# Kernel optimization log

Hardware: AMD Instinct MI355X
Metric: run time of the kernel (lower is better)

The kernel has to match this reference:

```python
import jax, jax.numpy as jnp
from jax import lax
import numpy as np
import math

D = 96   # d_model
H = 4    # num_heads (d_k = d_v = D per head, per the source)
K = 7    # depthwise kernel size
L = 4    # num conv layers


def _pos_encoding(seq_len, d):
    # Faithful to the source's (nonstandard) exponents: sin uses 2*i/d, cos uses 2*(i+1)/d
    pos = np.arange(seq_len, dtype=np.float32)[:, None]
    i = np.arange(0, d, 2, dtype=np.float32)
    pe = np.zeros((seq_len, d), dtype=np.float32)
    pe[:, 0::2] = np.sin(pos / 10000.0 ** (2.0 * i / d))
    pe[:, 1::2] = np.cos(pos / 10000.0 ** (2.0 * (i + 1.0) / d))
    return jnp.asarray(pe)


def _layernorm(x, g, b, eps=1e-5):
    m = jnp.mean(x, axis=-1, keepdims=True)
    v = jnp.mean((x - m) ** 2, axis=-1, keepdims=True)
    return (x - m) / jnp.sqrt(v + eps) * g + b


def setup_inputs() -> dict:
    key = jax.random.key(0)
    ks = jax.random.split(key, 10)
    B, S = 128, 384

    def xavier(k, shape, fan_in, fan_out):
        bound = math.sqrt(6.0 / (fan_in + fan_out))
        return jax.random.uniform(k, shape, jnp.float32, -bound, bound)

    return {
        "input": jax.random.normal(ks[0], (B, S, D), jnp.float32),
        "mask": jnp.zeros((B, S), dtype=bool),
        "conv_dw": jax.random.normal(ks[1], (L, D, 1, K), jnp.float32) * 0.05,
        "conv_dw_b": jnp.zeros((L, D), jnp.float32),
        "conv_pw": jax.random.normal(ks[2], (L, D, D, 1), jnp.float32) * 0.05,
        "conv_pw_b": jnp.zeros((L, D), jnp.float32),
        "WQ": xavier(ks[3], (H, D, D), D, D),
        "WK": xavier(ks[4], (H, D, D), D, D),
        "WV": xavier(ks[5], (H, D, D), D, D),
        "WO": xavier(ks[6], (H * D, D), H * D, D),
        "ffn_w1": jax.random.normal(ks[7], (D, D // 2), jnp.float32) * 0.1,
        "ffn_b1": jnp.zeros((D // 2,), jnp.float32),
        "ffn_w2": jax.random.normal(ks[8], (D // 2, D), jnp.float32) * 0.1,
        "ffn_b2": jnp.zeros((D,), jnp.float32),
        "ln_g": jnp.ones((L + 2, D), jnp.float32),
        "ln_b": jnp.zeros((L + 2, D), jnp.float32),
    }


def reference(input, mask, conv_dw, conv_dw_b, conv_pw, conv_pw_b,
              WQ, WK, WV, WO, ffn_w1, ffn_b1, ffn_w2, ffn_b2, ln_g, ln_b):
    B, S, _ = input.shape
    dn = ("NCH", "OIH", "NCH")

    # positional encoding (eval mode: all dropout is identity)
    x = input * jnp.float32(math.sqrt(D)) + _pos_encoding(S, D)[None]

    # conv blocks: LN -> depthwise conv -> pointwise conv -> relu -> residual
    for i in range(L):
        h = _layernorm(x, ln_g[i], ln_b[i])
        h = jnp.transpose(h, (0, 2, 1))  # [B, C, S]
        h = lax.conv_general_dilated(h, conv_dw[i], (1,), "SAME",
                                     feature_group_count=D, dimension_numbers=dn)
        h = h + conv_dw_b[i][None, :, None]
        h = lax.conv_general_dilated(h, conv_pw[i], (1,), "SAME", dimension_numbers=dn)
        h = jax.nn.relu(h + conv_pw_b[i][None, :, None])
        x = x + jnp.transpose(h, (0, 2, 1))

    # multi-head attention with per-head full-width projections (d_k = D)
    h = _layernorm(x, ln_g[L], ln_b[L])
    Q = jnp.einsum("bsd,hde->hbse", h, WQ)
    Kh = jnp.einsum("bsd,hde->hbse", h, WK)
    V = jnp.einsum("bsd,hde->hbse", h, WV)
    # source divides scores by temperature = 1/sqrt(d_k) => multiply by sqrt(D)
    scores = jnp.einsum("hbqe,hbke->hbqk", Q, Kh) * jnp.float32(math.sqrt(D))
    # mask is viewed [B, S, 1]: masks query rows, broadcast over keys
    scores = jnp.where(mask[None, :, :, None], -jnp.inf, scores)
    attn = jax.nn.softmax(scores, axis=-1)
    ctx = jnp.einsum("hbqk,hbke->hbqe", attn, V)
    cat = jnp.transpose(ctx, (1, 2, 0, 3)).reshape(B, S, H * D)
    x = x + cat @ WO

    # feed-forward: Linear -> sigmoid -> Linear, residual
    h2 = _layernorm(x, ln_g[L + 1], ln_b[L + 1])
    ff = jax.nn.sigmoid(h2 @ ffn_w1 + ffn_b1) @ ffn_w2 + ffn_b2
    return x + ff
```

## Files before the change

### kernel.cpp

```cpp
#include <hip/hip_runtime.h>
#include <math.h>


constexpr int B = 128;
constexpr int S = 384;
constexpr int D = 96;
constexpr int H = 4;
constexpr int KW = 7;
constexpr int L = 4;
constexpr int ROWS = B * S;
constexpr long long NTOT = (long long)ROWS * D;
constexpr float SQRTD = 9.797958971132712f;
constexpr float LOG2E = 1.4426950408889634f;

typedef _Float16 f16x8 __attribute__((ext_vector_type(8)));
typedef float f32x4 __attribute__((ext_vector_type(4)));
typedef unsigned short us;
typedef unsigned short us4 __attribute__((ext_vector_type(4)));
typedef unsigned short us8 __attribute__((ext_vector_type(8)));

__device__ __forceinline__ us f2h(float f) {
    _Float16 h = (_Float16)f;
    return __builtin_bit_cast(us, h);
}
__device__ __forceinline__ f16x8 ldh(const us* p) {
    return *reinterpret_cast<const f16x8*>(p);
}

__global__ void pe_kernel(float* __restrict__ pe) {
    int idx = blockIdx.x * 256 + threadIdx.x;
    if (idx >= S * D) return;
    int s = idx / D, c = idx - s * D;
    int j = c >> 1;
    float expo = (c & 1) ? (4.0f * j + 2.0f) / 96.0f : (4.0f * j) / 96.0f;
    float freq = expf(-expo * logf(10000.0f));
    float ang = (float)s * freq;
    pe[idx] = (c & 1) ? cosf(ang) : sinf(ang);
}

__global__ void prep_w(const float* __restrict__ WQ, const float* __restrict__ WK,
                       const float* __restrict__ cpw, const float* __restrict__ w1,
                       const float* __restrict__ w2,
                       us* __restrict__ wqS, us* __restrict__ wkS, us* __restrict__ pwS,
                       us* __restrict__ w1S, us* __restrict__ w2S) {
    int idx = blockIdx.x * 256 + threadIdx.x;
    if (idx >= H * D * D) return;
    int h = idx / (D * D), rem = idx - h * (D * D);
    int d = rem / D, e = rem - d * D;
    int n = e >> 4, lmod = e & 15, kk = d >> 5, ldiv = (d >> 3) & 3, j = d & 7;
    size_t fi = (size_t)(((n * 3 + kk) * 64 + ldiv * 16 + lmod) * 8 + j);
    wqS[(size_t)h * D * D + fi] = f2h(WQ[idx] * SQRTD * LOG2E);
    wkS[(size_t)h * D * D + fi] = f2h(WK[idx]);
    {
        int l = idx / (D * D);
        int o = rem / D, c = rem - o * D;
        int no = o >> 4, lo = o & 15, kc = c >> 5, lc = (c >> 3) & 3, jc = c & 7;
        pwS[(size_t)l * D * D + (size_t)(((no * 3 + kc) * 64 + lc * 16 + lo) * 8 + jc)] =
            f2h(cpw[idx]);
    }
    if (idx < 48 * 96) {
        int m = idx / 96, c = idx - m * 96;
        int nm = m >> 4, lm = m & 15, kc = c >> 5, lc = (c >> 3) & 3, jc = c & 7;
        w1S[((nm * 3 + kc) * 64 + lc * 16 + lm) * 8 + jc] = f2h(w1[c * 48 + m]);
    }
    if (idx < 96 * 64) {
        int o = idx / 64, mk = idx - o * 64;
        int no = o >> 4, lo = o & 15, km = mk >> 5, lm2 = (mk >> 3) & 3, jm = mk & 7;
        w2S[((no * 2 + km) * 64 + lm2 * 16 + lo) * 8 + jm] =
            (mk < 48) ? f2h(w2[mk * 96 + o]) : (us)0;
    }
}

__global__ void prep_wvo(const float* __restrict__ WV, const float* __restrict__ WO,
                         us* __restrict__ wvoS) {
    int blk = blockIdx.x;
    int h = blk / 6, ot = blk - h * 6;
    int tid = threadIdx.x;
    const float* wv = WV + (size_t)h * D * D;
    const float* wo = WO + (size_t)h * D * D;
    for (int i = tid; i < 16 * 96; i += 256) {
        int lmod = i / 96, d = i - (i / 96) * 96;
        int o = ot * 16 + lmod;
        float acc = 0.f;
        for (int e = 0; e < 96; e++) acc += wv[d * 96 + e] * wo[e * 96 + o];
        int kk = d >> 5, ldiv = (d >> 3) & 3, j = d & 7;
        wvoS[(size_t)h * D * D + (size_t)(((ot * 3 + kk) * 64 + ldiv * 16 + lmod) * 8 + j)] =
            f2h(acc);
    }
}

__global__ void conv0f(const float* __restrict__ in, const float* __restrict__ pe,
                       const float* __restrict__ g0, const float* __restrict__ b0,
                       float* __restrict__ xout, us* __restrict__ lnout,
                       const float* __restrict__ dwW, const float* __restrict__ dwB,
                       const us* __restrict__ pwW, const float* __restrict__ pwb,
                       const float* __restrict__ gnext, const float* __restrict__ bnext) {
    __shared__ us lnb_s[70 * 104];
    __shared__ us dwb_s[64 * 104];
    __shared__ float lw[96 * 8];
    int tid = threadIdx.x;
    int wave = tid >> 6, lane = tid & 63;
    int r0 = blockIdx.x * 64;
    int b = r0 / S, s0 = r0 % S;

    for (int i = tid; i < 96 * KW; i += 256) lw[(i / KW) * 8 + (i % KW)] = dwW[i];

    for (int i = wave; i < 70; i += 4) {
        int s = s0 - 3 + i;
        bool valid = (unsigned)s < (unsigned)S;
        float v0 = 0.f, v1 = 0.f;
        if (valid) {
            size_t ro = ((size_t)b * S + s) * 96;
            v0 = in[ro + lane] * SQRTD + pe[s * 96 + lane];
            v1 = (lane < 32) ? in[ro + 64 + lane] * SQRTD + pe[s * 96 + 64 + lane] : 0.f;
        }
        float sm = v0 + v1, q = v0 * v0 + v1 * v1;
        for (int off = 32; off > 0; off >>= 1) {
            sm += __shfl_xor(sm, off);
            q += __shfl_xor(q, off);
        }
        float mean = sm * (1.0f / D);
        float var = q * (1.0f / D) - mean * mean;
        float rstd = rsqrtf(var + 1e-5f);
        lnb_s[i * 104 + lane] = f2h(valid ? (v0 - mean) * rstd * g0[lane] + b0[lane] : 0.f);
        if (lane < 32)
            lnb_s[i * 104 + 64 + lane] =
                f2h(valid ? (v1 - mean) * rstd * g0[lane + 64] + b0[lane + 64] : 0.f);
    }
    __syncthreads();

    for (int u = tid; u < 768; u += 256) {
        int j = u / 12, c0 = (u - (u / 12) * 12) * 8;
        float acc[8];
        #pragma unroll
        for (int j2 = 0; j2 < 8; j2++) acc[j2] = dwB[c0 + j2];
        #pragma unroll
        for (int k = 0; k < KW; k++) {
            f16x8 v = ldh(&lnb_s[(j + k) * 104 + c0]);
            #pragma unroll
            for (int j2 = 0; j2 < 8; j2++) acc[j2] += (float)v[j2] * lw[(c0 + j2) * 8 + k];
        }
        us8 o;
        #pragma unroll
        for (int j2 = 0; j2 < 8; j2++) o[j2] = f2h(acc[j2]);
        *reinterpret_cast<us8*>(&dwb_s[j * 104 + c0]) = o;
    }
    __syncthreads();

    int lmod = lane & 15, ldiv = lane >> 4, m0 = wave * 16;
    f32x4 acc[6] = {};
    #pragma unroll
    for (int kk = 0; kk < 3; kk++) {
        f16x8 af = ldh(&dwb_s[(m0 + lmod) * 104 + kk * 32 + ldiv * 8]);
        #pragma unroll
        for (int n = 0; n < 6; n++) {
            f16x8 bf = ldh(pwW + (size_t)((n * 3 + kk) * 64) * 8 + lane * 8);
            acc[n] = __builtin_amdgcn_mfma_f32_16x16x32_f16(af, bf, acc[n], 0, 0, 0);
        }
    }

    float gv[6], bv2[6], pb[6];
    #pragma unroll
    for (int n = 0; n < 6; n++) {
        int o = n * 16 + lmod;
        gv[n] = gnext[o];
        bv2[n] = bnext[o];
        pb[n] = pwb[o];
    }
    #pragma unroll
    for (int n = 0; n < 6; n++) {
        int o = n * 16 + lmod;
        #pragma unroll
        for (int r = 0; r < 4; r++) {
            int sr = m0 + ldiv * 4 + r;
            size_t row = (size_t)r0 + sr;
            float base = in[row * 96 + o] * SQRTD + pe[(s0 + sr) * 96 + o];
            acc[n][r] = base + fmaxf(acc[n][r] + pb[n], 0.f);
        }
    }
    #pragma unroll
    for (int r = 0; r < 4; r++) {
        float sm = 0.f, qq = 0.f;
        #pragma unroll
        for (int n = 0; n < 6; n++) {
            sm += acc[n][r];
            qq += acc[n][r] * acc[n][r];
        }
        #pragma unroll
        for (int st = 1; st <= 8; st <<= 1) {
            sm += __shfl_xor(sm, st);
            qq += __shfl_xor(qq, st);
        }
        float mean = sm * (1.0f / D);
        float var = qq * (1.0f / D) - mean * mean;
        float rstd = rsqrtf(var + 1e-5f);
        size_t row = (size_t)r0 + m0 + ldiv * 4 + r;
        #pragma unroll
        for (int n = 0; n < 6; n++) {
            int o = n * 16 + lmod;
            xout[row * 96 + o] = acc[n][r];
            lnout[row * 96 + o] = f2h((acc[n][r] - mean) * rstd * gv[n] + bv2[n]);
        }
    }
}

__global__ void conv2(const float* __restrict__ xin, const us* __restrict__ lnin,
                      float* __restrict__ xout, us* __restrict__ lnout,
                      const float* __restrict__ dwW, const float* __restrict__ dwB,
                      const us* __restrict__ pwW, const float* __restrict__ pwb,
                      const float* __restrict__ gnext, const float* __restrict__ bnext) {
    __shared__ us dwb_s[64 * 104];
    __shared__ float lw[96 * 8];
    int tid = threadIdx.x;
    int wave = tid >> 6, lane = tid & 63;
    int r0 = blockIdx.x * 64;
    int b = r0 / S, s0 = r0 % S;

    for (int i = tid; i < 96 * KW; i += 256) lw[(i / KW) * 8 + (i % KW)] = dwW[i];
    __syncthreads();

    for (int u = tid; u < 768; u += 256) {
        int j = u / 12, c0 = (u - (u / 12) * 12) * 8;
        float acc[8];
        #pragma unroll
        for (int j2 = 0; j2 < 8; j2++) acc[j2] = dwB[c0 + j2];
        #pragma unroll
        for (int k = 0; k < KW; k++) {
            int ss = s0 + j + k - 3;
            if ((unsigned)ss < (unsigned)S) {
                f16x8 v = ldh(lnin + ((size_t)b * S + ss) * 96 + c0);
                #pragma unroll
                for (int j2 = 0; j2 < 8; j2++) acc[j2] += (float)v[j2] * lw[(c0 + j2) * 8 + k];
            }
        }
        us8 o;
        #pragma unroll
        for (int j2 = 0; j2 < 8; j2++) o[j2] = f2h(acc[j2]);
        *reinterpret_cast<us8*>(&dwb_s[j * 104 + c0]) = o;
    }
    __syncthreads();

    int lmod = lane & 15, ldiv = lane >> 4, m0 = wave * 16;
    f32x4 acc[6] = {};
    #pragma unroll
    for (int kk = 0; kk < 3; kk++) {
        f16x8 af = ldh(&dwb_s[(m0 + lmod) * 104 + kk * 32 + ldiv * 8]);
        #pragma unroll
        for (int n = 0; n < 6; n++) {
            f16x8 bf = ldh(pwW + (size_t)((n * 3 + kk) * 64) * 8 + lane * 8);
            acc[n] = __builtin_amdgcn_mfma_f32_16x16x32_f16(af, bf, acc[n], 0, 0, 0);
        }
    }

    float gv[6], bv2[6], pb[6];
    #pragma unroll
    for (int n = 0; n < 6; n++) {
        int o = n * 16 + lmod;
        gv[n] = gnext[o];
        bv2[n] = bnext[o];
        pb[n] = pwb[o];
    }
    #pragma unroll
    for (int n = 0; n < 6; n++) {
        #pragma unroll
        for (int r = 0; r < 4; r++) {
            size_t row = (size_t)r0 + m0 + ldiv * 4 + r;
            acc[n][r] = xin[row * 96 + n * 16 + lmod] + fmaxf(acc[n][r] + pb[n], 0.f);
        }
    }
    #pragma unroll
    for (int r = 0; r < 4; r++) {
        float sm = 0.f, qq = 0.f;
        #pragma unroll
        for (int n = 0; n < 6; n++) {
            sm += acc[n][r];
            qq += acc[n][r] * acc[n][r];
        }
        #pragma unroll
        for (int st = 1; st <= 8; st <<= 1) {
            sm += __shfl_xor(sm, st);
            qq += __shfl_xor(qq, st);
        }
        float mean = sm * (1.0f / D);
        float var = qq * (1.0f / D) - mean * mean;
        float rstd = rsqrtf(var + 1e-5f);
        size_t row = (size_t)r0 + m0 + ldiv * 4 + r;
        #pragma unroll
        for (int n = 0; n < 6; n++) {
            int o = n * 16 + lmod;
            xout[row * 96 + o] = acc[n][r];
            lnout[row * 96 + o] = f2h((acc[n][r] - mean) * rstd * gv[n] + bv2[n]);
        }
    }
}

__global__ void conv3p(const float* __restrict__ xin, const us* __restrict__ lnin,
                       float* __restrict__ xout, us* __restrict__ lnout,
                       const float* __restrict__ dwW, const float* __restrict__ dwB,
                       const us* __restrict__ pwW, const float* __restrict__ pwb,
                       const float* __restrict__ gnext, const float* __restrict__ bnext,
                       const us* __restrict__ wkS, const us* __restrict__ wvoS,
                       us* __restrict__ Kall, us* __restrict__ Vall) {
    __shared__ float lw[96 * 8];
    __shared__ us stg[96 * 72];
    __shared__ us lnstg[64 * 104];
    int tid = threadIdx.x;
    int wave = tid >> 6, lane = tid & 63;
    int lmod = lane & 15, ldiv = lane >> 4, m0 = wave * 16;
    int r0 = blockIdx.x * 64;
    int b = r0 / S, s0 = r0 % S;

    for (int i = tid; i < 96 * KW; i += 256) lw[(i / KW) * 8 + (i % KW)] = dwW[i];
    __syncthreads();

    for (int u = tid; u < 768; u += 256) {
        int j = u / 12, c0 = (u - (u / 12) * 12) * 8;
        float acc[8];
        #pragma unroll
        for (int j2 = 0; j2 < 8; j2++) acc[j2] = dwB[c0 + j2];
        #pragma unroll
        for (int k = 0; k < KW; k++) {
            int ss = s0 + j + k - 3;
            if ((unsigned)ss < (unsigned)S) {
                f16x8 v = ldh(lnin + ((size_t)b * S + ss) * 96 + c0);
                #pragma unroll
                for (int j2 = 0; j2 < 8; j2++) acc[j2] += (float)v[j2] * lw[(c0 + j2) * 8 + k];
            }
        }
        us8 o;
        #pragma unroll
        for (int j2 = 0; j2 < 8; j2++) o[j2] = f2h(acc[j2]);
        *reinterpret_cast<us8*>(&stg[j * 104 + c0]) = o;
    }
    __syncthreads();

    f32x4 acc[6] = {};
    #pragma unroll
    for (int kk = 0; kk < 3; kk++) {
        f16x8 af = ldh(&stg[(m0 + lmod) * 104 + kk * 32 + ldiv * 8]);
        #pragma unroll
        for (int n = 0; n < 6; n++) {
            f16x8 bf = ldh(pwW + (size_t)((n * 3 + kk) * 64) * 8 + lane * 8);
            acc[n] = __builtin_amdgcn_mfma_f32_16x16x32_f16(af, bf, acc[n], 0, 0, 0);
        }
    }

    float gv[6], bv2[6], pb[6];
    #pragma unroll
    for (int n = 0; n < 6; n++) {
        int o = n * 16 + lmod;
        gv[n] = gnext[o];
        bv2[n] = bnext[o];
        pb[n] = pwb[o];
    }
    #pragma unroll
    for (int n = 0; n < 6; n++) {
        #pragma unroll
        for (int r = 0; r < 4; r++) {
            size_t row = (size_t)r0 + m0 + ldiv * 4 + r;
            acc[n][r] = xin[row * 96 + n * 16 + lmod] + fmaxf(acc[n][r] + pb[n], 0.f);
        }
    }
    #pragma unroll
    for (int r = 0; r < 4; r++) {
        float sm = 0.f, qq = 0.f;
        #pragma unroll
        for (int n = 0; n < 6; n++) {
            sm += acc[n][r];
            qq += acc[n][r] * acc[n][r];
        }
        #pragma unroll
        for (int st = 1; st <= 8; st <<= 1) {
            sm += __shfl_xor(sm, st);
            qq += __shfl_xor(qq, st);
        }
        float mean = sm * (1.0f / D);
        float var = qq * (1.0f / D) - mean * mean;
        float rstd = rsqrtf(var + 1e-5f);
        size_t row = (size_t)r0 + m0 + ldiv * 4 + r;
        #pragma unroll
        for (int n = 0; n < 6; n++) {
            int o = n * 16 + lmod;
            xout[row * 96 + o] = acc[n][r];
            us hv = f2h((acc[n][r] - mean) * rstd * gv[n] + bv2[n]);
            lnout[row * 96 + o] = hv;
            lnstg[(m0 + ldiv * 4 + r) * 104 + o] = hv;
        }
    }
    __syncthreads();

    f16x8 af[3];
    #pragma unroll
    for (int kk = 0; kk < 3; kk++)
        af[kk] = ldh(&lnstg[(m0 + lmod) * 104 + kk * 32 + ldiv * 8]);

    for (int hd = 0; hd < H; hd++) {
        f32x4 ka[6] = {};
        #pragma unroll
        for (int kk = 0; kk < 3; kk++)
            #pragma unroll
            for (int n = 0; n < 6; n++) {
                f16x8 bf = ldh(wkS + (size_t)hd * D * D + (size_t)((n * 3 + kk) * 64) * 8 + lane * 8);
                ka[n] = __builtin_amdgcn_mfma_f32_16x16x32_f16(af[kk], bf, ka[n], 0, 0, 0);
            }
        __syncthreads();
        us* kT = stg + wave * 1664;
        #pragma unroll
        for (int n = 0; n < 6; n++)
            #pragma unroll
            for (int r = 0; r < 4; r++)
                kT[(ldiv * 4 + r) * 104 + n * 16 + lmod] = f2h(ka[n][r]);
        int t0 = (r0 % S) / 16 + wave;
        us* dst = Kall + (size_t)hd * NTOT + ((size_t)(b * 24 + t0) * 3) * 512;
        #pragma unroll
        for (int kk = 0; kk < 3; kk++) {
            us8 v = *reinterpret_cast<const us8*>(&kT[lmod * 104 + kk * 32 + ldiv * 8]);
            *reinterpret_cast<us8*>(dst + kk * 512 + lane * 8) = v;
        }
        f32x4 va[6] = {};
        #pragma unroll
        for (int kk = 0; kk < 3; kk++)
            #pragma unroll
            for (int n = 0; n < 6; n++) {
                f16x8 bf =
                    ldh(wvoS + (size_t)hd * D * D + (size_t)((n * 3 + kk) * 64) * 8 + lane * 8);
                va[n] = __builtin_amdgcn_mfma_f32_16x16x32_f16(af[kk], bf, va[n], 0, 0, 0);
            }
        __syncthreads();
        #pragma unroll
        for (int n = 0; n < 6; n++)
            #pragma unroll
            for (int r = 0; r < 4; r++)
                stg[(n * 16 + lmod) * 72 + m0 + ldiv * 4 + r] = f2h(va[n][r]);
        __syncthreads();
        int cblk = (r0 % S) / 64;
        us* dsth = Vall + (size_t)hd * NTOT;
        #pragma unroll
        for (int n = 0; n < 6; n++)
            #pragma unroll
            for (int kk = 0; kk < 2; kk++) {
                us8 v =
                    *reinterpret_cast<const us8*>(&stg[(n * 16 + lmod) * 72 + kk * 32 + ldiv * 8]);
                *reinterpret_cast<us8*>(
                    dsth + ((size_t)((b * 6 + cblk) * 6 + n) * 2 + kk) * 512 + lane * 8) = v;
            }
    }
}

__global__ __launch_bounds__(256, 2) void attn_g(const us* __restrict__ h16,
                                                 const us* __restrict__ wqS,
                                                 const us* __restrict__ Kall,
                                                 const us* __restrict__ Vall,
                                                 us* __restrict__ xpart) {
    __shared__ us pool[38400];
    int tid = threadIdx.x, wave = tid >> 6, lane = tid & 63;
    int lmod = lane & 15, ldiv = lane >> 4;
    int p = blockIdx.x;
    int gl = (p & 7) * 128 + (p >> 3);
    int qt = gl & 1;
    int bh = gl >> 1;
    int b = bh >> 2, hd = bh & 3;
    size_t rowbase = (size_t)b * S + qt * 192 + wave * 48;

    const us* Kh = Kall + (size_t)hd * NTOT + (size_t)b * 24 * 1536;
    const us* Vh = Vall + (size_t)hd * NTOT + (size_t)b * 36 * 1024;
    us* P = pool + 24576 + wave * 3456;

    us8 k0s[3];
    #pragma unroll
    for (int j = 0; j < 3; j++)
        k0s[j] = *reinterpret_cast<const us8*>(Kh + (size_t)(j * 256 + tid) * 8);

    f32x4 qa0[6] = {}, qa1[6] = {}, qa2[6] = {};
    #pragma unroll
    for (int kk = 0; kk < 3; kk++) {
        f16x8 a0 = ldh(h16 + (rowbase + lmod) * 96 + kk * 32 + ldiv * 8);
        f16x8 a1 = ldh(h16 + (rowbase + 16 + lmod) * 96 + kk * 32 + ldiv * 8);
        f16x8 a2 = ldh(h16 + (rowbase + 32 + lmod) * 96 + kk * 32 + ldiv * 8);
        #pragma unroll
        for (int n = 0; n < 6; n++) {
            f16x8 bf = ldh(wqS + (size_t)hd * D * D + (size_t)((n * 3 + kk) * 64) * 8 + lane * 8);
            qa0[n] = __builtin_amdgcn_mfma_f32_16x16x32_f16(a0, bf, qa0[n], 0, 0, 0);
            qa1[n] = __builtin_amdgcn_mfma_f32_16x16x32_f16(a1, bf, qa1[n], 0, 0, 0);
            qa2[n] = __builtin_amdgcn_mfma_f32_16x16x32_f16(a2, bf, qa2[n], 0, 0, 0);
        }
    }
    us* qst = pool + wave * 4992;
    #pragma unroll
    for (int n = 0; n < 6; n++)
        #pragma unroll
        for (int r = 0; r < 4; r++) {
            qst[(ldiv * 4 + r) * 104 + n * 16 + lmod] = f2h(qa0[n][r]);
            qst[(16 + ldiv * 4 + r) * 104 + n * 16 + lmod] = f2h(qa1[n][r]);
            qst[(32 + ldiv * 4 + r) * 104 + n * 16 + lmod] = f2h(qa2[n][r]);
        }
    f16x8 aq0[3], aq1[3], aq2[3];
    #pragma unroll
    for (int kk = 0; kk < 3; kk++) {
        aq0[kk] = ldh(&qst[lmod * 104 + kk * 32 + ldiv * 8]);
        aq1[kk] = ldh(&qst[(16 + lmod) * 104 + kk * 32 + ldiv * 8]);
        aq2[kk] = ldh(&qst[(32 + lmod) * 104 + kk * 32 + ldiv * 8]);
    }
    __syncthreads();
    #pragma unroll
    for (int j = 0; j < 3; j++)
        *reinterpret_cast<us8*>(&pool[(j * 256 + tid) * 8]) = k0s[j];
    __syncthreads();

    float mx0 = -1e30f, mx1 = -1e30f, mx2 = -1e30f;
    for (int c = 0; c < 6; c++) {
        us* kbc = pool + (c & 1) * 6144;
        us8 kn[3], vn[3];
        bool last = (c == 5);
        if (!last) {
            const us* src = Kh + (size_t)(c + 1) * 6144;
            #pragma unroll
            for (int j = 0; j < 3; j++)
                kn[j] = *reinterpret_cast<const us8*>(src + (size_t)(j * 256 + tid) * 8);
        } else {
            #pragma unroll
            for (int j = 0; j < 3; j++) {
                kn[j] = *reinterpret_cast<const us8*>(Kh + (size_t)(j * 256 + tid) * 8);
                vn[j] = *reinterpret_cast<const us8*>(Vh + (size_t)(j * 256 + tid) * 8);
            }
        }
        __builtin_amdgcn_s_setprio(1);
        f32x4 s0[4] = {}, s1[4] = {}, s2[4] = {};
        #pragma unroll
        for (int nt = 0; nt < 4; nt++)
            #pragma unroll
            for (int kk = 0; kk < 3; kk++) {
                f16x8 bf = ldh(&kbc[(nt * 3 + kk) * 512 + lane * 8]);
                s0[nt] = __builtin_amdgcn_mfma_f32_16x16x32_f16(bf, aq0[kk], s0[nt], 0, 0, 0);
                s1[nt] = __builtin_amdgcn_mfma_f32_16x16x32_f16(bf, aq1[kk], s1[nt], 0, 0, 0);
                s2[nt] = __builtin_amdgcn_mfma_f32_16x16x32_f16(bf, aq2[kk], s2[nt], 0, 0, 0);
            }
        __builtin_amdgcn_s_setprio(0);
        #pragma unroll
        for (int nt = 0; nt < 4; nt++)
            #pragma unroll
            for (int r = 0; r < 4; r++) {
                mx0 = fmaxf(mx0, s0[nt][r]);
                mx1 = fmaxf(mx1, s1[nt][r]);
                mx2 = fmaxf(mx2, s2[nt][r]);
            }
        us* kbw = pool + (last ? 0 : ((c & 1) ^ 1)) * 6144;
        #pragma unroll
        for (int j = 0; j < 3; j++)
            *reinterpret_cast<us8*>(&kbw[(j * 256 + tid) * 8]) = kn[j];
        if (last) {
            #pragma unroll
            for (int j = 0; j < 3; j++)
                *reinterpret_cast<us8*>(&pool[12288 + (j * 256 + tid) * 8]) = vn[j];
        }
        __syncthreads();
    }
    mx0 = fmaxf(mx0, __shfl_xor(mx0, 16));
    mx0 = fmaxf(mx0, __shfl_xor(mx0, 32));
    mx1 = fmaxf(mx1, __shfl_xor(mx1, 16));
    mx1 = fmaxf(mx1, __shfl_xor(mx1, 32));
    mx2 = fmaxf(mx2, __shfl_xor(mx2, 16));
    mx2 = fmaxf(mx2, __shfl_xor(mx2, 32));

    f32x4 oacc0[6] = {}, oacc1[6] = {}, oacc2[6] = {};
    float l0 = 0.f, l1 = 0.f, l2 = 0.f;
    for (int c = 0; c < 6; c++) {
        us* kbc = pool + (c & 1) * 6144;
        us* vbc = pool + 12288 + (c & 1) * 6144;
        us8 kn[3], vn[3];
        if (c < 5) {
            const us* ksrc = Kh + (size_t)(c + 1) * 6144;
            const us* vsrc = Vh + (size_t)(c + 1) * 6144;
            #pragma unroll
            for (int j = 0; j < 3; j++) {
                kn[j] = *reinterpret_cast<const us8*>(ksrc + (size_t)(j * 256 + tid) * 8);
                vn[j] = *reinterpret_cast<const us8*>(vsrc + (size_t)(j * 256 + tid) * 8);
            }
        }
        __builtin_amdgcn_s_setprio(1);
        f32x4 s0[4] = {}, s1[4] = {}, s2[4] = {};
        #pragma unroll
        for (int nt = 0; nt < 4; nt++)
            #pragma unroll
            for (int kk = 0; kk < 3; kk++) {
                f16x8 bf = ldh(&kbc[(nt * 3 + kk) * 512 + lane * 8]);
                s0[nt] = __builtin_amdgcn_mfma_f32_16x16x32_f16(bf, aq0[kk], s0[nt], 0, 0, 0);
                s1[nt] = __builtin_amdgcn_mfma_f32_16x16x32_f16(bf, aq1[kk], s1[nt], 0, 0, 0);
                s2[nt] = __builtin_amdgcn_mfma_f32_16x16x32_f16(bf, aq2[kk], s2[nt], 0, 0, 0);
            }
        __builtin_amdgcn_s_setprio(0);
        #pragma unroll
        for (int nt = 0; nt < 4; nt++) {
            us4 pk0, pk1, pk2;
            #pragma unroll
            for (int r = 0; r < 4; r++) {
                float p0 = exp2f(s0[nt][r] - mx0);
                float p1 = exp2f(s1[nt][r] - mx1);
                float p2 = exp2f(s2[nt][r] - mx2);
                l0 += p0;
                l1 += p1;
                l2 += p2;
                pk0[r] = f2h(p0);
                pk1[r] = f2h(p1);
                pk2[r] = f2h(p2);
            }
            int kc = nt * 16 + ldiv * 4;
            *reinterpret_cast<us4*>(&P[lmod * 72 + kc]) = pk0;
            *reinterpret_cast<us4*>(&P[(16 + lmod) * 72 + kc]) = pk1;
            *reinterpret_cast<us4*>(&P[(32 + lmod) * 72 + kc]) = pk2;
        }
        __builtin_amdgcn_s_setprio(1);
        #pragma unroll
        for (int kk = 0; kk < 2; kk++) {
            f16x8 pf0 = ldh(&P[lmod * 72 + kk * 32 + ldiv * 8]);
            f16x8 pf1 = ldh(&P[(16 + lmod) * 72 + kk * 32 + ldiv * 8]);
            f16x8 pf2 = ldh(&P[(32 + lmod) * 72 + kk * 32 + ldiv * 8]);
            #pragma unroll
            for (int n = 0; n < 6; n++) {
                f16x8 bf = ldh(&vbc[(n * 2 + kk) * 512 + lane * 8]);
                oacc0[n] = __builtin_amdgcn_mfma_f32_16x16x32_f16(pf0, bf, oacc0[n], 0, 0, 0);
                oacc1[n] = __builtin_amdgcn_mfma_f32_16x16x32_f16(pf1, bf, oacc1[n], 0, 0, 0);
                oacc2[n] = __builtin_amdgcn_mfma_f32_16x16x32_f16(pf2, bf, oacc2[n], 0, 0, 0);
            }
        }
        __builtin_amdgcn_s_setprio(0);
        if (c < 5) {
            us* kbn = pool + ((c & 1) ^ 1) * 6144;
            us* vbn = pool + 12288 + ((c & 1) ^ 1) * 6144;
            #pragma unroll
            for (int j = 0; j < 3; j++) {
                *reinterpret_cast<us8*>(&kbn[(j * 256 + tid) * 8]) = kn[j];
                *reinterpret_cast<us8*>(&vbn[(j * 256 + tid) * 8]) = vn[j];
            }
            __syncthreads();
        }
    }
    l0 += __shfl_xor(l0, 16);
    l0 += __shfl_xor(l0, 32);
    l1 += __shfl_xor(l1, 16);
    l1 += __shfl_xor(l1, 32);
    l2 += __shfl_xor(l2, 16);
    l2 += __shfl_xor(l2, 32);

    us* xp = xpart + (size_t)hd * NTOT;
    #pragma unroll
    for (int r = 0; r < 4; r++) {
        int srcl = ldiv * 4 + r;
        float inv0 = 1.f / __shfl(l0, srcl);
        float inv1 = 1.f / __shfl(l1, srcl);
        float inv2 = 1.f / __shfl(l2, srcl);
        #pragma unroll
        for (int n = 0; n < 6; n++) {
            xp[(rowbase + ldiv * 4 + r) * 96 + n * 16 + lmod] = f2h(oacc0[n][r] * inv0);
            xp[(rowbase + 16 + ldiv * 4 + r) * 96 + n * 16 + lmod] = f2h(oacc1[n][r] * inv1);
            xp[(rowbase + 32 + ldiv * 4 + r) * 96 + n * 16 + lmod] = f2h(oacc2[n][r] * inv2);
        }
    }
}

__global__ void ffn_ln(const float* __restrict__ x, const us* __restrict__ xpart,
                       const float* __restrict__ gln, const float* __restrict__ bln,
                       const us* __restrict__ w1S, const float* __restrict__ b1,
                       const us* __restrict__ w2S, const float* __restrict__ b2,
                       float* __restrict__ out) {
    __shared__ float xf[64 * 96];
    __shared__ us lnb[64 * 104];
    __shared__ us mid[64 * 72];
    int tid = threadIdx.x, wave = tid >> 6, lane = tid & 63;
    int lmod = lane & 15, ldiv = lane >> 4, m0 = wave * 16;
    int row0 = blockIdx.x * 64;

    for (int i = wave; i < 64; i += 4) {
        size_t ro = (size_t)(row0 + i) * 96;
        float v0 = x[ro + lane];
        float v1 = (lane < 32) ? x[ro + 64 + lane] : 0.f;
        #pragma unroll
        for (int h = 0; h < H; h++) {
            const us* xp = xpart + (size_t)h * NTOT + ro;
            v0 += (float)__builtin_bit_cast(_Float16, xp[lane]);
            if (lane < 32) v1 += (float)__builtin_bit_cast(_Float16, xp[64 + lane]);
        }
        xf[i * 96 + lane] = v0;
        if (lane < 32) xf[i * 96 + 64 + lane] = v1;
        float sm = v0 + v1, q = v0 * v0 + v1 * v1;
        for (int off = 32; off > 0; off >>= 1) {
            sm += __shfl_xor(sm, off);
            q += __shfl_xor(q, off);
        }
        float mean = sm * (1.0f / D);
        float var = q * (1.0f / D) - mean * mean;
        float rstd = rsqrtf(var + 1e-5f);
        lnb[i * 104 + lane] = f2h((v0 - mean) * rstd * gln[lane] + bln[lane]);
        if (lane < 32)
            lnb[i * 104 + 64 + lane] = f2h((v1 - mean) * rstd * gln[lane + 64] + bln[lane + 64]);
    }
    __syncthreads();

    f32x4 a3[3] = {};
    #pragma unroll
    for (int kk = 0; kk < 3; kk++) {
        f16x8 af = ldh(&lnb[(m0 + lmod) * 104 + kk * 32 + ldiv * 8]);
        #pragma unroll
        for (int n = 0; n < 3; n++) {
            f16x8 bf = ldh(w1S + (size_t)((n * 3 + kk) * 64) * 8 + lane * 8);
            a3[n] = __builtin_amdgcn_mfma_f32_16x16x32_f16(af, bf, a3[n], 0, 0, 0);
        }
    }
    #pragma unroll
    for (int n = 0; n < 3; n++) {
        float bv = b1[n * 16 + lmod];
        #pragma unroll
        for (int r = 0; r < 4; r++) {
            float v = a3[n][r] + bv;
            mid[(m0 + ldiv * 4 + r) * 72 + n * 16 + lmod] = f2h(1.f / (1.f + __expf(-v)));
        }
    }
    #pragma unroll
    for (int r = 0; r < 4; r++) mid[(m0 + ldiv * 4 + r) * 72 + 48 + lmod] = 0;
    __syncthreads();

    f32x4 a6[6] = {};
    #pragma unroll
    for (int kk = 0; kk < 2; kk++) {
        f16x8 af = ldh(&mid[(m0 + lmod) * 72 + kk * 32 + ldiv * 8]);
        #pragma unroll
        for (int n = 0; n < 6; n++) {
            f16x8 bf = ldh(w2S + (size_t)((n * 2 + kk) * 64) * 8 + lane * 8);
            a6[n] = __builtin_amdgcn_mfma_f32_16x16x32_f16(af, bf, a6[n], 0, 0, 0);
        }
    }
    #pragma unroll
    for (int n = 0; n < 6; n++) {
        int o = n * 16 + lmod;
        float bv = b2[o];
        #pragma unroll
        for (int r = 0; r < 4; r++) {
            int sr = m0 + ldiv * 4 + r;
            out[(size_t)(row0 + sr) * 96 + o] = xf[sr * 96 + o] + a6[n][r] + bv;
        }
    }
}

extern "C" void kernel_launch(void* const* d_in, const int* in_sizes, int n_in,
                              void* d_out, int out_size, void* d_ws, size_t ws_size,
                              hipStream_t stream) {
    const float* in   = (const float*)d_in[0];
    const float* cdw  = (const float*)d_in[2];
    const float* cdwb = (const float*)d_in[3];
    const float* cpw  = (const float*)d_in[4];
    const float* cpwb = (const float*)d_in[5];
    const float* WQ   = (const float*)d_in[6];
    const float* WK   = (const float*)d_in[7];
    const float* WV   = (const float*)d_in[8];
    const float* WO   = (const float*)d_in[9];
    const float* w1   = (const float*)d_in[10];
    const float* b1   = (const float*)d_in[11];
    const float* w2   = (const float*)d_in[12];
    const float* b2   = (const float*)d_in[13];
    const float* lng  = (const float*)d_in[14];
    const float* lnb  = (const float*)d_in[15];
    float* out = (float*)d_out;
    float* ws = (float*)d_ws;

    float* xA  = ws;
    float* xB  = xA + NTOT;
    float* pe  = xB + NTOT;
    us* lnA    = (us*)(pe + S * D);
    us* lnB    = lnA + NTOT;
    us* Kall   = lnB + NTOT;
    us* Vall   = Kall + (size_t)H * NTOT;
    us* xpart  = Vall + (size_t)H * NTOT;
    us* wqS    = xpart + (size_t)H * NTOT;
    us* wkS    = wqS + H * D * D;
    us* wvoS   = wkS + H * D * D;
    us* pwS    = wvoS + H * D * D;
    us* w1S    = pwS + L * D * D;
    us* w2S    = w1S + 48 * 96;

    pe_kernel<<<(S * D + 255) / 256, 256, 0, stream>>>(pe);
    prep_w<<<(H * D * D + 255) / 256, 256, 0, stream>>>(WQ, WK, cpw, w1, w2,
                                                        wqS, wkS, pwS, w1S, w2S);
    prep_wvo<<<H * 6, 256, 0, stream>>>(WV, WO, wvoS);

    conv0f<<<ROWS / 64, 256, 0, stream>>>(in, pe, lng, lnb, xA, lnB,
                                          cdw, cdwb, pwS, cpwb, lng + D, lnb + D);
    conv2<<<ROWS / 64, 256, 0, stream>>>(xA, lnB, xB, lnA, cdw + D * KW, cdwb + D,
                                         pwS + D * D, cpwb + D, lng + 2 * D, lnb + 2 * D);
    conv2<<<ROWS / 64, 256, 0, stream>>>(xB, lnA, xA, lnB, cdw + 2 * D * KW, cdwb + 2 * D,
                                         pwS + 2 * D * D, cpwb + 2 * D, lng + 3 * D,
                                         lnb + 3 * D);
    conv3p<<<ROWS / 64, 256, 0, stream>>>(xA, lnB, xB, lnA, cdw + 3 * D * KW, cdwb + 3 * D,
                                          pwS + 3 * D * D, cpwb + 3 * D, lng + 4 * D,
                                          lnb + 4 * D, wkS, wvoS, Kall, Vall);

    attn_g<<<1024, 256, 0, stream>>>(lnA, wqS, Kall, Vall, xpart);

    ffn_ln<<<ROWS / 64, 256, 0, stream>>>(xB, xpart, lng + 5 * D, lnb + 5 * D,
                                          w1S, b1, w2S, b2, out);
}
```

Baseline: 274.6 us.

## Replace two-pass softmax with single-pass online softmax in attention kernel

Removes the separate first pass over all key chunks that computed the row maximum, and instead keeps a running maximum with rescaling of the accumulated sum and output, as in flash attention. This halves the QK^T MFMA work and the K loads and LDS traffic for that pass. In exchange each chunk adds cross-lane shuffles for the chunk max and the per-row scale factors, plus multiplies to rescale the output accumulators. The first V chunk is now prefetched alongside the first K chunk.

Result: no change. 272.8 us (-0.7%).

```diff
diff --git a/kernel.cpp b/kernel.cpp
--- a/kernel.cpp
+++ b/kernel.cpp
@@ -466,10 +466,12 @@
     const us* Vh = Vall + (size_t)hd * NTOT + (size_t)b * 36 * 1024;
     us* P = pool + 24576 + wave * 3456;
 
-    us8 k0s[3];
-    #pragma unroll
-    for (int j = 0; j < 3; j++)
+    us8 k0s[3], v0s[3];
+    #pragma unroll
+    for (int j = 0; j < 3; j++) {
         k0s[j] = *reinterpret_cast<const us8*>(Kh + (size_t)(j * 256 + tid) * 8);
+        v0s[j] = *reinterpret_cast<const us8*>(Vh + (size_t)(j * 256 + tid) * 8);
+    }
 
     f32x4 qa0[6] = {}, qa1[6] = {}, qa2[6] = {};
     #pragma unroll
@@ -503,67 +505,15 @@
     }
     __syncthreads();
     #pragma unroll
-    for (int j = 0; j < 3; j++)
+    for (int j = 0; j < 3; j++) {
         *reinterpret_cast<us8*>(&pool[(j * 256 + tid) * 8]) = k0s[j];
-    __syncthreads();
-
-    float mx0 = -1e30f, mx1 = -1e30f, mx2 = -1e30f;
-    for (int c = 0; c < 6; c++) {
-        us* kbc = pool + (c & 1) * 6144;
-        us8 kn[3], vn[3];
-        bool last = (c == 5);
-        if (!last) {
-            const us* src = Kh + (size_t)(c + 1) * 6144;
-            #pragma unroll
-            for (int j = 0; j < 3; j++)
-                kn[j] = *reinterpret_cast<const us8*>(src + (size_t)(j * 256 + tid) * 8);
-        } else {
-            #pragma unroll
-            for (int j = 0; j < 3; j++) {
-                kn[j] = *reinterpret_cast<const us8*>(Kh + (size_t)(j * 256 + tid) * 8);
-                vn[j] = *reinterpret_cast<const us8*>(Vh + (size_t)(j * 256 + tid) * 8);
-            }
-        }
-        __builtin_amdgcn_s_setprio(1);
-        f32x4 s0[4] = {}, s1[4] = {}, s2[4] = {};
-        #pragma unroll
-        for (int nt = 0; nt < 4; nt++)
-            #pragma unroll
-            for (int kk = 0; kk < 3; kk++) {
-                f16x8 bf = ldh(&kbc[(nt * 3 + kk) * 512 + lane * 8]);
-                s0[nt] = __builtin_amdgcn_mfma_f32_16x16x32_f16(bf, aq0[kk], s0[nt], 0, 0, 0);
-                s1[nt] = __builtin_amdgcn_mfma_f32_16x16x32_f16(bf, aq1[kk], s1[nt], 0, 0, 0);
-                s2[nt] = __builtin_amdgcn_mfma_f32_16x16x32_f16(bf, aq2[kk], s2[nt], 0, 0, 0);
-            }
-        __builtin_amdgcn_s_setprio(0);
-        #pragma unroll
-        for (int nt = 0; nt < 4; nt++)
-            #pragma unroll
-            for (int r = 0; r < 4; r++) {
-                mx0 = fmaxf(mx0, s0[nt][r]);
-                mx1 = fmaxf(mx1, s1[nt][r]);
-                mx2 = fmaxf(mx2, s2[nt][r]);
-            }
-        us* kbw = pool + (last ? 0 : ((c & 1) ^ 1)) * 6144;
-        #pragma unroll
-        for (int j = 0; j < 3; j++)
-            *reinterpret_cast<us8*>(&kbw[(j * 256 + tid) * 8]) = kn[j];
-        if (last) {
-            #pragma unroll
-            for (int j = 0; j < 3; j++)
-                *reinterpret_cast<us8*>(&pool[12288 + (j * 256 + tid) * 8]) = vn[j];
-        }
-        __syncthreads();
-    }
-    mx0 = fmaxf(mx0, __shfl_xor(mx0, 16));
-    mx0 = fmaxf(mx0, __shfl_xor(mx0, 32));
-    mx1 = fmaxf(mx1, __shfl_xor(mx1, 16));
-    mx1 = fmaxf(mx1, __shfl_xor(mx1, 32));
-    mx2 = fmaxf(mx2, __shfl_xor(mx2, 16));
-    mx2 = fmaxf(mx2, __shfl_xor(mx2, 32));
-
+        *reinterpret_cast<us8*>(&pool[12288 + (j * 256 + tid) * 8]) = v0s[j];
+    }
+    __syncthreads();
+
+    float m0v = -1e30f, m1v = -1e30f, m2v = -1e30f;
+    float l0 = 0.f, l1 = 0.f, l2 = 0.f;
     f32x4 oacc0[6] = {}, oacc1[6] = {}, oacc2[6] = {};
-    float l0 = 0.f, l1 = 0.f, l2 = 0.f;
     for (int c = 0; c < 6; c++) {
         us* kbc = pool + (c & 1) * 6144;
         us* vbc = pool + 12288 + (c & 1) * 6144;
@@ -589,14 +539,50 @@
                 s2[nt] = __builtin_amdgcn_mfma_f32_16x16x32_f16(bf, aq2[kk], s2[nt], 0, 0, 0);
             }
         __builtin_amdgcn_s_setprio(0);
+        float cm0 = -1e30f, cm1 = -1e30f, cm2 = -1e30f;
+        #pragma unroll
+        for (int nt = 0; nt < 4; nt++)
+            #pragma unroll
+            for (int r = 0; r < 4; r++) {
+                cm0 = fmaxf(cm0, s0[nt][r]);
+                cm1 = fmaxf(cm1, s1[nt][r]);
+                cm2 = fmaxf(cm2, s2[nt][r]);
+            }
+        cm0 = fmaxf(cm0, __shfl_xor(cm0, 16));
+        cm0 = fmaxf(cm0, __shfl_xor(cm0, 32));
+        cm1 = fmaxf(cm1, __shfl_xor(cm1, 16));
+        cm1 = fmaxf(cm1, __shfl_xor(cm1, 32));
+        cm2 = fmaxf(cm2, __shfl_xor(cm2, 16));
+        cm2 = fmaxf(cm2, __shfl_xor(cm2, 32));
+        float mn0 = fmaxf(m0v, cm0), mn1 = fmaxf(m1v, cm1), mn2 = fmaxf(m2v, cm2);
+        float sc0 = exp2f(m0v - mn0), sc1 = exp2f(m1v - mn1), sc2 = exp2f(m2v - mn2);
+        m0v = mn0;
+        m1v = mn1;
+        m2v = mn2;
+        l0 *= sc0;
+        l1 *= sc1;
+        l2 *= sc2;
+        #pragma unroll
+        for (int r = 0; r < 4; r++) {
+            int srcl = ldiv * 4 + r;
+            float s0r = __shfl(sc0, srcl);
+            float s1r = __shfl(sc1, srcl);
+            float s2r = __shfl(sc2, srcl);
+            #pragma unroll
+            for (int n = 0; n < 6; n++) {
+                oacc0[n][r] *= s0r;
+                oacc1[n][r] *= s1r;
+                oacc2[n][r] *= s2r;
+            }
+        }
         #pragma unroll
         for (int nt = 0; nt < 4; nt++) {
             us4 pk0, pk1, pk2;
             #pragma unroll
             for (int r = 0; r < 4; r++) {
-                float p0 = exp2f(s0[nt][r] - mx0);
-                float p1 = exp2f(s1[nt][r] - mx1);
-                float p2 = exp2f(s2[nt][r] - mx2);
+                float p0 = exp2f(s0[nt][r] - m0v);
+                float p1 = exp2f(s1[nt][r] - m1v);
+                float p2 = exp2f(s2[nt][r] - m2v);
                 l0 += p0;
                 l1 += p1;
                 l2 += p2;
```
